# Kernel optimization log

Hardware: AMD Instinct MI355X
Metric: run time of the kernel (lower is better)

The kernel has to match this reference:

```python
import jax, jax.numpy as jnp
import numpy as np

TAU = [1, 2, 4, 8]
B, T, FC, FX = 128, 2048, 512, 512


def setup_inputs() -> dict:
    key = jax.random.key(0)
    k1, k2, k3, k4 = jax.random.split(key, 4)
    C = jax.random.normal(k1, (B, T, FC), dtype=jnp.float32)
    X = jax.random.normal(k2, (B, T, FX), dtype=jnp.float32)
    # one Linear(encoding_size -> context_size) per tau; torch weight layout [out, in]
    W = jax.random.normal(k3, (len(TAU), FC, FX), dtype=jnp.float32) * (1.0 / np.sqrt(FX))
    b = jax.random.normal(k4, (len(TAU), FC), dtype=jnp.float32) * 0.01
    return {"C": C, "X": X, "W": W, "b": b}


def _infonce(Ct, Xe, Wk, bk):
    # Ct: [B, Tt, fc], Xe: [B, Tt, fx]
    Xt = jnp.einsum('btf,gf->btg', Xe, Wk) + bk          # Linear: [B, Tt, fc]
    Z = jnp.einsum('itf,jtf->ijt', Ct, Xt)               # scores [B, B, Tt]
    Zmax = jnp.max(Z, axis=1, keepdims=True)             # [B, 1, Tt]
    lse = jnp.log(jnp.sum(jnp.exp(Z - Zmax), axis=1)) + Zmax[:, 0]  # [B, Tt]
    Zdiag = jnp.diagonal(Z, axis1=0, axis2=1).T          # Z[i,i,t] -> [B, Tt]
    return jnp.mean(Zdiag - lse)


def reference(C, X, W, b):
    losses = [_infonce(C[:, :-t], X[:, t:], W[k], b[k]) for k, t in enumerate(TAU)]
    return jnp.stack(losses)
```

## Files before the change

### kernel.cpp

```cpp
#include <hip/hip_runtime.h>
#include <math.h>

constexpr int Tn  = 2048;
constexpr int FCn = 512;
constexpr int FXn = 512;
constexpr int SXW = 72;
constexpr int SYC = 136;
constexpr int SZS = 132;

typedef __attribute__((ext_vector_type(8))) short  bf16x8;
typedef __attribute__((ext_vector_type(4))) float  f32x4;

__device__ __forceinline__ unsigned pk2(float a, float b) {
  return __builtin_amdgcn_perm(__float_as_uint(b), __float_as_uint(a), 0x07060302u);
}
__device__ __forceinline__ uint4 pack8(float4 a, float4 b) {
  uint4 rv;
  rv.x = pk2(a.x, a.y); rv.y = pk2(a.z, a.w);
  rv.z = pk2(b.x, b.y); rv.w = pk2(b.z, b.w);
  return rv;
}

__device__ __forceinline__ void gll16(const unsigned short* g, void* lds) {
  __builtin_amdgcn_global_load_lds(
      (const __attribute__((address_space(1))) unsigned int*)g,
      (__attribute__((address_space(3))) unsigned int*)lds, 16, 0, 0);
}

__global__ void zero4(float* out) {
  if (threadIdx.x < 4) out[threadIdx.x] = 0.0f;
}

__global__ void finalize4(float* out) {
  int k = threadIdx.x;
  if (k < 4) out[k] *= 1.0f / (128.0f * (float)(Tn - (1 << k)));
}

__global__ void tobf16(const float* __restrict__ s, unsigned short* __restrict__ d) {
  int i = blockIdx.x * 256 + threadIdx.x;
  float4 v = ((const float4*)s)[i];
  uint2 p; p.x = pk2(v.x, v.y); p.y = pk2(v.z, v.w);
  ((uint2*)d)[i] = p;
}

__global__ __launch_bounds__(256, 2)
void infonce_v9(const float* __restrict__ Cp, const unsigned short* __restrict__ Xb,
                const unsigned short* __restrict__ Wb, float* __restrict__ out)
{
  __shared__ __align__(16) unsigned char smem[67648];
  char* sm = (char*)smem;
  float* sZ   = (float*)sm;
  float* sRed = (float*)(sm + 67584);

  const int tid = threadIdx.x;
  const int l   = tid & 63;
  const int w   = tid >> 6;
  const int r   = l & 15;
  const int h   = l >> 4;
  const int jw  = w >> 1;
  const int gw  = w & 1;
  const int iw  = w >> 1;
  const int jw2 = w & 1;

  const int orig = blockIdx.x;
  const int xcd  = orig & 7;
  const int loc  = orig >> 3;
  const int wg   = (xcd < 4) ? (xcd * 1024 + loc) : (4096 + (xcd - 4) * 1023 + loc);
  const int k    = wg & 3;
  const int t    = wg >> 2;
  const int tau  = 1 << k;
  if (t >= Tn - tau) return;
  const int s = t + tau;

  const int sub = l >> 2;
  const int gsw = (l & 3) ^ ((l >> 3) & 3);
  const size_t xstr = (size_t)Tn * FXn;
  const unsigned short* xs0 = Xb + (size_t)(w * 32 + sub) * xstr
                              + (size_t)s * FXn + gsw * 8;
  const unsigned short* xs1 = xs0 + (size_t)16 * xstr;
  const unsigned short* wk  = Wb + (size_t)k * (FCn * FXn) + gsw * 8;
  const unsigned short* ws0 = wk  + (size_t)(w * 64 + sub) * FXn;
  const unsigned short* ws1 = ws0 + (size_t)16 * FXn;
  const unsigned short* ws2 = ws0 + (size_t)32 * FXn;
  const unsigned short* ws3 = ws0 + (size_t)48 * FXn;

  const size_t cstr = (size_t)Tn * FCn;
  const float* cr0 = Cp + (size_t)(iw * 64 +  0 + r) * cstr + (size_t)t * FCn;
  const float* cr1 = Cp + (size_t)(iw * 64 + 16 + r) * cstr + (size_t)t * FCn;
  const float* cr2 = Cp + (size_t)(iw * 64 + 32 + r) * cstr + (size_t)t * FCn;
  const float* cr3 = Cp + (size_t)(iw * 64 + 48 + r) * cstr + (size_t)t * FCn;

  f32x4 zacc[4][4];
#pragma unroll
  for (int a = 0; a < 4; ++a)
#pragma unroll
    for (int b = 0; b < 4; ++b) zacc[a][b] = f32x4{0.f, 0.f, 0.f, 0.f};

#define STG8(BUFC, XC) do { \
    char* _bb = sm + (BUFC) * 24576; \
    const size_t _xo = (size_t)(XC) * 32; \
    gll16(xs0 + _xo, _bb + (w * 2    ) * 1024); \
    gll16(xs1 + _xo, _bb + (w * 2 + 1) * 1024); \
    const size_t _wo = wgc + _xo; \
    gll16(ws0 + _wo, _bb + 8192 + (w * 4    ) * 1024); \
    gll16(ws1 + _wo, _bb + 8192 + (w * 4 + 1) * 1024); \
    gll16(ws2 + _wo, _bb + 8192 + (w * 4 + 2) * 1024); \
    gll16(ws3 + _wo, _bb + 8192 + (w * 4 + 3) * 1024); \
  } while (0)

#define MFY8(BUFC) do { \
    const char* _bx = sm + (BUFC) * 24576; \
    const char* _bw = _bx + 8192; \
    const int _gb = (h ^ ((r >> 1) & 3)) << 4; \
    bf16x8 _ax[4]; \
    _Pragma("unroll") \
    for (int _bm = 0; _bm < 4; ++_bm) \
      _ax[_bm] = *(const bf16x8*)(_bx + (jw * 64 + _bm * 16 + r) * 64 + _gb); \
    bf16x8 _bv[8]; \
    _Pragma("unroll") \
    for (int _bn = 0; _bn < 8; ++_bn) \
      _bv[_bn] = *(const bf16x8*)(_bw + (gw * 128 + _bn * 16 + r) * 64 + _gb); \
    _Pragma("unroll") \
    for (int _bm = 0; _bm < 4; ++_bm) \
      _Pragma("unroll") \
      for (int _bn = 0; _bn < 8; ++_bn) \
        yacc[_bm][_bn] = __builtin_amdgcn_mfma_f32_16x16x32_bf16( \
            _ax[_bm], _bv[_bn], yacc[_bm][_bn], 0, 0, 0); \
  } while (0)

#pragma unroll 1
  for (int gc = 0; gc < 2; ++gc) {
    const size_t wgc = (size_t)gc * 256 * FXn;
    f32x4 yacc[4][8];
#pragma unroll
    for (int a = 0; a < 4; ++a)
#pragma unroll
      for (int b = 0; b < 8; ++b) yacc[a][b] = f32x4{0.f, 0.f, 0.f, 0.f};

    STG8(0, 0);
    __syncthreads();
#pragma unroll 1
    for (int xc2 = 0; xc2 < 8; ++xc2) {
      STG8(1, 2 * xc2 + 1);
      MFY8(0);
      __syncthreads();
      if (xc2 < 7) STG8(0, 2 * xc2 + 2);
      MFY8(1);
      __syncthreads();
    }

#pragma unroll
    for (int bm = 0; bm < 4; ++bm)
#pragma unroll
      for (int bn = 0; bn < 8; ++bn)
#pragma unroll
        for (int reg = 0; reg < 4; ++reg) {
          const int row = jw * 64 + bm * 16 + h * 4 + reg;
          const int col = gw * 128 + bn * 16 + r;
          *(unsigned short*)(sm + row * 528 + col * 2) =
              (unsigned short)(__float_as_uint(yacc[bm][bn][reg]) >> 16);
        }
    __syncthreads();

#pragma unroll 2
    for (int ks2 = 0; ks2 < 8; ++ks2) {
      const int goff = gc * 256 + ks2 * 32 + h * 8;
      float4 u0 = *(const float4*)(cr0 + goff), p0 = *(const float4*)(cr0 + goff + 4);
      float4 u1 = *(const float4*)(cr1 + goff), p1 = *(const float4*)(cr1 + goff + 4);
      float4 u2 = *(const float4*)(cr2 + goff), p2 = *(const float4*)(cr2 + goff + 4);
      float4 u3 = *(const float4*)(cr3 + goff), p3 = *(const float4*)(cr3 + goff + 4);
      bf16x8 acv[4];
      acv[0] = __builtin_bit_cast(bf16x8, pack8(u0, p0));
      acv[1] = __builtin_bit_cast(bf16x8, pack8(u1, p1));
      acv[2] = __builtin_bit_cast(bf16x8, pack8(u2, p2));
      acv[3] = __builtin_bit_cast(bf16x8, pack8(u3, p3));
      const int gb = ks2 * 64 + h * 16;
      bf16x8 byv[4];
#pragma unroll
      for (int bn = 0; bn < 4; ++bn)
        byv[bn] = *(const bf16x8*)(sm + (jw2 * 64 + bn * 16 + r) * 528 + gb);
#pragma unroll
      for (int bm = 0; bm < 4; ++bm)
#pragma unroll
        for (int bn = 0; bn < 4; ++bn)
          zacc[bm][bn] = __builtin_amdgcn_mfma_f32_16x16x32_bf16(
              acv[bm], byv[bn], zacc[bm][bn], 0, 0, 0);
    }
    __syncthreads();
  }

#pragma unroll
  for (int bm = 0; bm < 4; ++bm)
#pragma unroll
    for (int bn = 0; bn < 4; ++bn)
#pragma unroll
      for (int reg = 0; reg < 4; ++reg)
        sZ[(iw * 64 + bm * 16 + h * 4 + reg) * SZS + (jw2 * 64 + bn * 16 + r)] =
            zacc[bm][bn][reg];
  __syncthreads();

  const int row = w * 32 + (l >> 1);
  const int c0l = l & 1;
  float mx = -3.4e38f;
#pragma unroll
  for (int m = 0; m < 64; ++m) mx = fmaxf(mx, sZ[row * SZS + c0l + m * 2]);
  mx = fmaxf(mx, __shfl_xor(mx, 1));
  float sum = 0.f;
#pragma unroll
  for (int m = 0; m < 64; ++m) sum += __expf(sZ[row * SZS + c0l + m * 2] - mx);
  sum += __shfl_xor(sum, 1);
  float val = (c0l == 0) ? (sZ[row * SZS + row] - (__logf(sum) + mx)) : 0.f;
#pragma unroll
  for (int off = 1; off < 64; off <<= 1) val += __shfl_xor(val, off);
  if (l == 0) sRed[w] = val;
  __syncthreads();
  if (tid == 0) atomicAdd(out + k, sRed[0] + sRed[1] + sRed[2] + sRed[3]);
#undef STG8
#undef MFY8
}

template <bool WBF>
__global__ __launch_bounds__(512, 4)
void infonce_main(const float* __restrict__ Cp, const float* __restrict__ Xp,
                  const void* __restrict__ Wp, float* __restrict__ out)
{
  __shared__ __align__(16) unsigned char smem[71680];
  unsigned short* sX = (unsigned short*)(smem);
  unsigned short* sW = (unsigned short*)(smem + 18432);
  unsigned short* sY = (unsigned short*)(smem + 36864);
  unsigned short* sC = (unsigned short*)(smem);
  float* sZ   = (float*)(smem);
  float* sRed = (float*)(smem + 67584);

  const int tid  = threadIdx.x;
  const int lane = tid & 63;
  const int wave = tid >> 6;
  const int r    = lane & 15;
  const int h    = lane >> 4;
  const int wr   = wave >> 1;
  const int wc   = wave & 1;

  const int orig = blockIdx.x;
  const int xcd  = orig & 7;
  const int loc  = orig >> 3;
  const int wg   = (xcd < 4) ? (xcd * 1024 + loc) : (4096 + (xcd - 4) * 1023 + loc);
  const int k    = wg & 3;
  const int t    = wg >> 2;
  const int tau  = 1 << k;
  if (t >= Tn - tau) return;

  const float* Cb = Cp + (size_t)t * FCn;
  const float* Xb = Xp + (size_t)(t + tau) * FXn;

  const int srow = tid >> 2;
  const int scol = (tid & 3) * 16;
  const float* xs = Xb + (size_t)srow * (Tn * FXn) + scol;
  unsigned short* xd = sX + srow * SXW + scol;
  unsigned short* wd = sW + srow * SXW + scol;
  const unsigned short* wsh = (const unsigned short*)Wp + (size_t)k * (FCn * FXn)
                              + (size_t)srow * FXn + scol;
  const float* wsf = (const float*)Wp + (size_t)k * (FCn * FXn)
                     + (size_t)srow * FXn + scol;
  const int crow0 = tid >> 4;
  const int ccol  = (tid & 15) * 8;
  const float* cs = Cb + (size_t)crow0 * (Tn * FCn) + ccol;
  unsigned short* cd = sC + crow0 * SYC + ccol;
  const size_t cstep = (size_t)32 * Tn * FCn;

  float4 px0, px1, px2, px3;
  float4 pw0, pw1, pw2, pw3;
  uint4  pb0, pb1;
  float4 pc0, pc1, pc2, pc3, pc4, pc5, pc6, pc7;

#define LOAD_X(XC) do { \
    const float4* _p = (const float4*)(xs + (XC) * 64); \
    px0 = _p[0]; px1 = _p[1]; px2 = _p[2]; px3 = _p[3]; } while (0)
#define LOAD_W(GC, XC) do { \
    if constexpr (WBF) { \
      const uint4* _p = (const uint4*)(wsh + (size_t)((GC) * 128) * FXn + (XC) * 64); \
      pb0 = _p[0]; pb1 = _p[1]; \
    } else { \
      const float4* _p = (const float4*)(wsf + (size_t)((GC) * 128) * FXn + (XC) * 64); \
      pw0 = _p[0]; pw1 = _p[1]; pw2 = _p[2]; pw3 = _p[3]; } } while (0)
#define STORE_XW() do { \
    *(uint4*)(xd)     = pack8(px0, px1); \
    *(uint4*)(xd + 8) = pack8(px2, px3); \
    if constexpr (WBF) { *(uint4*)(wd) = pb0; *(uint4*)(wd + 8) = pb1; } \
    else { *(uint4*)(wd) = pack8(pw0, pw1); *(uint4*)(wd + 8) = pack8(pw2, pw3); } \
  } while (0)
#define MFMA_YF() do { \
    _Pragma("unroll") \
    for (int ks = 0; ks < 2; ++ks) { \
      const int xoo = ks * 32 + h * 8; \
      bf16x8 a0 = *(const bf16x8*)(sX + (wr * 32 + 0  + r) * SXW + xoo); \
      bf16x8 a1 = *(const bf16x8*)(sX + (wr * 32 + 16 + r) * SXW + xoo); \
      _Pragma("unroll") \
      for (int bg = 0; bg < 4; ++bg) { \
        bf16x8 bb = *(const bf16x8*)(sW + (wc * 64 + bg * 16 + r) * SXW + xoo); \
        yacc[0][bg] = __builtin_amdgcn_mfma_f32_16x16x32_bf16(a0, bb, yacc[0][bg], 0, 0, 0); \
        yacc[1][bg] = __builtin_amdgcn_mfma_f32_16x16x32_bf16(a1, bb, yacc[1][bg], 0, 0, 0); \
      } } } while (0)

  f32x4 zacc[2][4];
#pragma unroll
  for (int a = 0; a < 2; ++a)
#pragma unroll
    for (int b = 0; b < 4; ++b) zacc[a][b] = f32x4{0.f, 0.f, 0.f, 0.f};

  LOAD_X(0); LOAD_W(0, 0);

  for (int gc = 0; gc < 4; ++gc) {
    f32x4 yacc[2][4];
#pragma unroll
    for (int a = 0; a < 2; ++a)
#pragma unroll
      for (int b = 0; b < 4; ++b) yacc[a][b] = f32x4{0.f, 0.f, 0.f, 0.f};

    for (int xc = 0; xc < 7; ++xc) {
      __syncthreads();
      STORE_XW();
      __syncthreads();
      LOAD_X(xc + 1); LOAD_W(gc, xc + 1);
      MFMA_YF();
    }
    __syncthreads();
    STORE_XW();
    __syncthreads();
    {
      const float4* p0 = (const float4*)(cs + 0 * cstep + gc * 128);
      const float4* p1 = (const float4*)(cs + 1 * cstep + gc * 128);
      const float4* p2 = (const float4*)(cs + 2 * cstep + gc * 128);
      const float4* p3 = (const float4*)(cs + 3 * cstep + gc * 128);
      pc0 = p0[0]; pc1 = p0[1];
      pc2 = p1[0]; pc3 = p1[1];
      pc4 = p2[0]; pc5 = p2[1];
      pc6 = p3[0]; pc7 = p3[1];
    }
    MFMA_YF();

#pragma unroll
    for (int aj = 0; aj < 2; ++aj)
#pragma unroll
      for (int bg = 0; bg < 4; ++bg)
#pragma unroll
        for (int reg = 0; reg < 4; ++reg)
          sY[(wr * 32 + aj * 16 + h * 4 + reg) * SYC + (wc * 64 + bg * 16 + r)] =
              (unsigned short)(__float_as_uint(yacc[aj][bg][reg]) >> 16);
    __syncthreads();
    *(uint4*)(cd + 0 * 32 * SYC) = pack8(pc0, pc1);
    *(uint4*)(cd + 1 * 32 * SYC) = pack8(pc2, pc3);
    *(uint4*)(cd + 2 * 32 * SYC) = pack8(pc4, pc5);
    *(uint4*)(cd + 3 * 32 * SYC) = pack8(pc6, pc7);
    __syncthreads();
    if (gc < 3) { LOAD_X(0); LOAD_W(gc + 1, 0); }
#pragma unroll
    for (int ks = 0; ks < 4; ++ks) {
      const int go = ks * 32 + h * 8;
      bf16x8 a0 = *(const bf16x8*)(sC + (wr * 32 + 0  + r) * SYC + go);
      bf16x8 a1 = *(const bf16x8*)(sC + (wr * 32 + 16 + r) * SYC + go);
#pragma unroll
      for (int bj = 0; bj < 4; ++bj) {
        bf16x8 bb = *(const bf16x8*)(sY + (wc * 64 + bj * 16 + r) * SYC + go);
        zacc[0][bj] = __builtin_amdgcn_mfma_f32_16x16x32_bf16(a0, bb, zacc[0][bj], 0, 0, 0);
        zacc[1][bj] = __builtin_amdgcn_mfma_f32_16x16x32_bf16(a1, bb, zacc[1][bj], 0, 0, 0);
      }
    }
  }
  __syncthreads();
#pragma unroll
  for (int ai = 0; ai < 2; ++ai)
#pragma unroll
    for (int bj = 0; bj < 4; ++bj)
#pragma unroll
      for (int reg = 0; reg < 4; ++reg)
        sZ[(wr * 32 + ai * 16 + h * 4 + reg) * SZS + (wc * 64 + bj * 16 + r)] =
            zacc[ai][bj][reg];
  __syncthreads();

  const int row = wave * 16 + (lane >> 2);
  const int c0l = lane & 3;
  float mx = -3.4e38f;
#pragma unroll
  for (int m = 0; m < 32; ++m) mx = fmaxf(mx, sZ[row * SZS + c0l + m * 4]);
  mx = fmaxf(mx, __shfl_xor(mx, 1));
  mx = fmaxf(mx, __shfl_xor(mx, 2));
  float sum = 0.f;
#pragma unroll
  for (int m = 0; m < 32; ++m) sum += __expf(sZ[row * SZS + c0l + m * 4] - mx);
  sum += __shfl_xor(sum, 1);
  sum += __shfl_xor(sum, 2);
  float val = (c0l == 0) ? (sZ[row * SZS + row] - (__logf(sum) + mx)) : 0.f;
#pragma unroll
  for (int off = 1; off < 64; off <<= 1) val += __shfl_xor(val, off);
  if (lane == 0) sRed[wave] = val;
  __syncthreads();
  if (tid == 0) {
    float bs = 0.f;
#pragma unroll
    for (int w2 = 0; w2 < 8; ++w2) bs += sRed[w2];
    atomicAdd(out + k, bs);
  }
#undef LOAD_X
#undef LOAD_W
#undef STORE_XW
#undef MFMA_YF
}

extern "C" void kernel_launch(void* const* d_in, const int* in_sizes, int n_in,
                              void* d_out, int out_size, void* d_ws, size_t ws_size,
                              hipStream_t stream) {
  const float* C = (const float*)d_in[0];
  const float* X = (const float*)d_in[1];
  const float* W = (const float*)d_in[2];
  float* out = (float*)d_out;

  const size_t NX = (size_t)128 * Tn * FXn;
  const size_t NW = (size_t)4 * FCn * FXn;
  const size_t WS_W   = NW * 2;
  const size_t WS_MID = WS_W + NX * 2;

  hipLaunchKernelGGL(zero4, dim3(1), dim3(64), 0, stream, out);

  if (ws_size >= WS_MID) {
    unsigned short* Wbf = (unsigned short*)d_ws;
    unsigned short* Xbf = (unsigned short*)((char*)d_ws + WS_W);
    hipLaunchKernelGGL(tobf16, dim3((unsigned)(NW / 1024)), dim3(256), 0, stream, W, Wbf);
    hipLaunchKernelGGL(tobf16, dim3((unsigned)(NX / 1024)), dim3(256), 0, stream, X, Xbf);
    hipLaunchKernelGGL(infonce_v9, dim3(2047 * 4), dim3(256), 0, stream,
                       C, Xbf, Wbf, out);
  } else if (ws_size >= WS_W) {
    hipLaunchKernelGGL(tobf16, dim3((unsigned)(NW / 1024)), dim3(256), 0, stream,
                       W, (unsigned short*)d_ws);
    hipLaunchKernelGGL(infonce_main<true>, dim3(2047 * 4), dim3(512), 0, stream,
                       C, X, (const void*)d_ws, out);
  } else {
    hipLaunchKernelGGL(infonce_main<false>, dim3(2047 * 4), dim3(512), 0, stream,
                       C, X, (const void*)W, out);
  }
  hipLaunchKernelGGL(finalize4, dim3(1), dim3(64), 0, stream, out);
}
```

Baseline: 1.532 ms.

## Split InfoNCE tile across eight waves and read X operands straight from global

The fused InfoNCE kernel now runs 512 threads (eight waves) per block instead of 256. Each wave owns a 32-row slice of the batch instead of 64, which halves the per-wave accumulator tiles. Only W is staged through LDS, in wider 64-column chunks with an XOR swizzle. X fragments are loaded directly from global memory into registers for the MFMA A operand, and the Y and softmax reductions are re-split across the extra waves. The aim is more latency hiding and less LDS staging traffic, at the cost of redundant global X reads by paired waves and fewer k-steps per synchronisation.

```diff
diff --git a/kernel.cpp b/kernel.cpp
--- a/kernel.cpp
+++ b/kernel.cpp
@@ -7,6 +7,7 @@
 constexpr int SXW = 72;
 constexpr int SYC = 136;
 constexpr int SZS = 132;
+constexpr int SYB = 520;
 
 typedef __attribute__((ext_vector_type(8))) short  bf16x8;
 typedef __attribute__((ext_vector_type(4))) float  f32x4;
@@ -43,9 +44,9 @@
   ((uint2*)d)[i] = p;
 }
 
-__global__ __launch_bounds__(256, 2)
-void infonce_v9(const float* __restrict__ Cp, const unsigned short* __restrict__ Xb,
-                const unsigned short* __restrict__ Wb, float* __restrict__ out)
+__global__ __launch_bounds__(512, 4)
+void infonce_v10(const float* __restrict__ Cp, const unsigned short* __restrict__ Xb,
+                 const unsigned short* __restrict__ Wb, float* __restrict__ out)
 {
   __shared__ __align__(16) unsigned char smem[67648];
   char* sm = (char*)smem;
@@ -72,151 +73,136 @@
   if (t >= Tn - tau) return;
   const int s = t + tau;
 
-  const int sub = l >> 2;
-  const int gsw = (l & 3) ^ ((l >> 3) & 3);
   const size_t xstr = (size_t)Tn * FXn;
-  const unsigned short* xs0 = Xb + (size_t)(w * 32 + sub) * xstr
-                              + (size_t)s * FXn + gsw * 8;
-  const unsigned short* xs1 = xs0 + (size_t)16 * xstr;
-  const unsigned short* wk  = Wb + (size_t)k * (FCn * FXn) + gsw * 8;
-  const unsigned short* ws0 = wk  + (size_t)(w * 64 + sub) * FXn;
-  const unsigned short* ws1 = ws0 + (size_t)16 * FXn;
-  const unsigned short* ws2 = ws0 + (size_t)32 * FXn;
-  const unsigned short* ws3 = ws0 + (size_t)48 * FXn;
+  const unsigned short* xr0 = Xb + (size_t)(jw * 32 +  0 + r) * xstr + (size_t)s * FXn;
+  const unsigned short* xr1 = xr0 + (size_t)16 * xstr;
+
+  const int gsw8 = ((l & 7) ^ (l >> 3)) * 8;
+  const unsigned short* wbase = Wb + (size_t)k * (FCn * FXn);
 
   const size_t cstr = (size_t)Tn * FCn;
-  const float* cr0 = Cp + (size_t)(iw * 64 +  0 + r) * cstr + (size_t)t * FCn;
-  const float* cr1 = Cp + (size_t)(iw * 64 + 16 + r) * cstr + (size_t)t * FCn;
-  const float* cr2 = Cp + (size_t)(iw * 64 + 32 + r) * cstr + (size_t)t * FCn;
-  const float* cr3 = Cp + (size_t)(iw * 64 + 48 + r) * cstr + (size_t)t * FCn;
-
-  f32x4 zacc[4][4];
-#pragma unroll
-  for (int a = 0; a < 4; ++a)
+  const float* cr0 = Cp + (size_t)(iw * 32 +  0 + r) * cstr + (size_t)t * FCn;
+  const float* cr1 = cr0 + (size_t)16 * cstr;
+
+  f32x4 zacc[2][4];
+#pragma unroll
+  for (int a = 0; a < 2; ++a)
 #pragma unroll
     for (int b = 0; b < 4; ++b) zacc[a][b] = f32x4{0.f, 0.f, 0.f, 0.f};
 
-#define STG8(BUFC, XC) do { \
-    char* _bb = sm + (BUFC) * 24576; \
-    const size_t _xo = (size_t)(XC) * 32; \
-    gll16(xs0 + _xo, _bb + (w * 2    ) * 1024); \
-    gll16(xs1 + _xo, _bb + (w * 2 + 1) * 1024); \
-    const size_t _wo = wgc + _xo; \
-    gll16(ws0 + _wo, _bb + 8192 + (w * 4    ) * 1024); \
-    gll16(ws1 + _wo, _bb + 8192 + (w * 4 + 1) * 1024); \
-    gll16(ws2 + _wo, _bb + 8192 + (w * 4 + 2) * 1024); \
-    gll16(ws3 + _wo, _bb + 8192 + (w * 4 + 3) * 1024); \
+#define STG10(BUF, GC, XC) do { \
+    char* _bb = sm + (BUF) * 32768 + (w * 32) * 128; \
+    const unsigned short* _ws = wbase \
+        + (size_t)((GC) * 256 + w * 32 + (l >> 3)) * FXn + (XC) * 64 + gsw8; \
+    gll16(_ws,                    _bb); \
+    gll16(_ws + (size_t)8  * FXn, _bb + 1024); \
+    gll16(_ws + (size_t)16 * FXn, _bb + 2048); \
+    gll16(_ws + (size_t)24 * FXn, _bb + 3072); \
   } while (0)
 
-#define MFY8(BUFC) do { \
-    const char* _bx = sm + (BUFC) * 24576; \
-    const char* _bw = _bx + 8192; \
-    const int _gb = (h ^ ((r >> 1) & 3)) << 4; \
-    bf16x8 _ax[4]; \
+#define MFY10(BUF, XC) do { \
+    const char* _bw = sm + (BUF) * 32768; \
     _Pragma("unroll") \
-    for (int _bm = 0; _bm < 4; ++_bm) \
-      _ax[_bm] = *(const bf16x8*)(_bx + (jw * 64 + _bm * 16 + r) * 64 + _gb); \
-    bf16x8 _bv[8]; \
-    _Pragma("unroll") \
-    for (int _bn = 0; _bn < 8; ++_bn) \
-      _bv[_bn] = *(const bf16x8*)(_bw + (gw * 128 + _bn * 16 + r) * 64 + _gb); \
-    _Pragma("unroll") \
-    for (int _bm = 0; _bm < 4; ++_bm) \
+    for (int _ks = 0; _ks < 2; ++_ks) { \
+      const int _xo = (XC) * 64 + _ks * 32 + h * 8; \
+      bf16x8 _a0 = *(const bf16x8*)(xr0 + _xo); \
+      bf16x8 _a1 = *(const bf16x8*)(xr1 + _xo); \
+      const int _cb = (_ks * 64 + h * 16) ^ ((r & 7) << 4); \
       _Pragma("unroll") \
-      for (int _bn = 0; _bn < 8; ++_bn) \
-        yacc[_bm][_bn] = __builtin_amdgcn_mfma_f32_16x16x32_bf16( \
-            _ax[_bm], _bv[_bn], yacc[_bm][_bn], 0, 0, 0); \
+      for (int _bn = 0; _bn < 8; ++_bn) { \
+        bf16x8 _bv = *(const bf16x8*)(_bw + (gw * 128 + _bn * 16 + r) * 128 + _cb); \
+        yacc[0][_bn] = __builtin_amdgcn_mfma_f32_16x16x32_bf16(_a0, _bv, yacc[0][_bn], 0, 0, 0); \
+        yacc[1][_bn] = __builtin_amdgcn_mfma_f32_16x16x32_bf16(_a1, _bv, yacc[1][_bn], 0, 0, 0); \
+      } \
+    } \
   } while (0)
 
 #pragma unroll 1
   for (int gc = 0; gc < 2; ++gc) {
-    const size_t wgc = (size_t)gc * 256 * FXn;
-    f32x4 yacc[4][8];
-#pragma unroll
-    for (int a = 0; a < 4; ++a)
+    f32x4 yacc[2][8];
+#pragma unroll
+    for (int a = 0; a < 2; ++a)
 #pragma unroll
       for (int b = 0; b < 8; ++b) yacc[a][b] = f32x4{0.f, 0.f, 0.f, 0.f};
 
-    STG8(0, 0);
+    STG10(0, gc, 0);
     __syncthreads();
 #pragma unroll 1
-    for (int xc2 = 0; xc2 < 8; ++xc2) {
-      STG8(1, 2 * xc2 + 1);
-      MFY8(0);
+    for (int p2 = 0; p2 < 4; ++p2) {
+      STG10(1, gc, 2 * p2 + 1);
+      MFY10(0, 2 * p2);
       __syncthreads();
-      if (xc2 < 7) STG8(0, 2 * xc2 + 2);
-      MFY8(1);
+      if (p2 < 3) STG10(0, gc, 2 * p2 + 2);
+      MFY10(1, 2 * p2 + 1);
       __syncthreads();
     }
 
 #pragma unroll
-    for (int bm = 0; bm < 4; ++bm)
+    for (int bm = 0; bm < 2; ++bm)
 #pragma unroll
       for (int bn = 0; bn < 8; ++bn)
 #pragma unroll
         for (int reg = 0; reg < 4; ++reg) {
-          const int row = jw * 64 + bm * 16 + h * 4 + reg;
+          const int row = jw * 32 + bm * 16 + h * 4 + reg;
           const int col = gw * 128 + bn * 16 + r;
-          *(unsigned short*)(sm + row * 528 + col * 2) =
+          *(unsigned short*)(sm + row * SYB + col * 2) =
               (unsigned short)(__float_as_uint(yacc[bm][bn][reg]) >> 16);
         }
     __syncthreads();
 
 #pragma unroll 2
     for (int ks2 = 0; ks2 < 8; ++ks2) {
-      const int goff = gc * 256 + ks2 * 32 + h * 8;
-      float4 u0 = *(const float4*)(cr0 + goff), p0 = *(const float4*)(cr0 + goff + 4);
-      float4 u1 = *(const float4*)(cr1 + goff), p1 = *(const float4*)(cr1 + goff + 4);
-      float4 u2 = *(const float4*)(cr2 + goff), p2 = *(const float4*)(cr2 + goff + 4);
-      float4 u3 = *(const float4*)(cr3 + goff), p3 = *(const float4*)(cr3 + goff + 4);
-      bf16x8 acv[4];
-      acv[0] = __builtin_bit_cast(bf16x8, pack8(u0, p0));
-      acv[1] = __builtin_bit_cast(bf16x8, pack8(u1, p1));
-      acv[2] = __builtin_bit_cast(bf16x8, pack8(u2, p2));
-      acv[3] = __builtin_bit_cast(bf16x8, pack8(u3, p3));
-      const int gb = ks2 * 64 + h * 16;
-      bf16x8 byv[4];
-#pragma unroll
-      for (int bn = 0; bn < 4; ++bn)
-        byv[bn] = *(const bf16x8*)(sm + (jw2 * 64 + bn * 16 + r) * 528 + gb);
-#pragma unroll
-      for (int bm = 0; bm < 4; ++bm)
-#pragma unroll
-        for (int bn = 0; bn < 4; ++bn)
-          zacc[bm][bn] = __builtin_amdgcn_mfma_f32_16x16x32_bf16(
-              acv[bm], byv[bn], zacc[bm][bn], 0, 0, 0);
+      const int gcol = gc * 256 + ks2 * 32 + h * 8;
+      float4 u0 = *(const float4*)(cr0 + gcol), p0 = *(const float4*)(cr0 + gcol + 4);
+      float4 u1 = *(const float4*)(cr1 + gcol), p1 = *(const float4*)(cr1 + gcol + 4);
+      bf16x8 a0 = __builtin_bit_cast(bf16x8, pack8(u0, p0));
+      bf16x8 a1 = __builtin_bit_cast(bf16x8, pack8(u1, p1));
+      const int yb = ks2 * 64 + h * 16;
+#pragma unroll
+      for (int bn = 0; bn < 4; ++bn) {
+        bf16x8 bv = *(const bf16x8*)(sm + (jw2 * 64 + bn * 16 + r) * SYB + yb);
+        zacc[0][bn] = __builtin_amdgcn_mfma_f32_16x16x32_bf16(a0, bv, zacc[0][bn], 0, 0, 0);
+        zacc[1][bn] = __builtin_amdgcn_mfma_f32_16x16x32_bf16(a1, bv, zacc[1][bn], 0, 0, 0);
+      }
     }
     __syncthreads();
   }
 
 #pragma unroll
-  for (int bm = 0; bm < 4; ++bm)
+  for (int bm = 0; bm < 2; ++bm)
 #pragma unroll
     for (int bn = 0; bn < 4; ++bn)
 #pragma unroll
       for (int reg = 0; reg < 4; ++reg)
-        sZ[(iw * 64 + bm * 16 + h * 4 + reg) * SZS + (jw2 * 64 + bn * 16 + r)] =
+        sZ[(iw * 32 + bm * 16 + h * 4 + reg) * SZS + (jw2 * 64 + bn * 16 + r)] =
             zacc[bm][bn][reg];
   __syncthreads();
 
-  const int row = w * 32 + (l >> 1);
-  const int c0l = l & 1;
+  const int row = w * 16 + (l >> 2);
+  const int c0l = l & 3;
   float mx = -3.4e38f;
 #pragma unroll
-  for (int m = 0; m < 64; ++m) mx = fmaxf(mx, sZ[row * SZS + c0l + m * 2]);
+  for (int m = 0; m < 32; ++m) mx = fmaxf(mx, sZ[row * SZS + c0l + m * 4]);
   mx = fmaxf(mx, __shfl_xor(mx, 1));
+  mx = fmaxf(mx, __shfl_xor(mx, 2));
   float sum = 0.f;
 #pragma unroll
-  for (int m = 0; m < 64; ++m) sum += __expf(sZ[row * SZS + c0l + m * 2] - mx);
+  for (int m = 0; m < 32; ++m) sum += __expf(sZ[row * SZS + c0l + m * 4] - mx);
   sum += __shfl_xor(sum, 1);
+  sum += __shfl_xor(sum, 2);
   float val = (c0l == 0) ? (sZ[row * SZS + row] - (__logf(sum) + mx)) : 0.f;
 #pragma unroll
   for (int off = 1; off < 64; off <<= 1) val += __shfl_xor(val, off);
   if (l == 0) sRed[w] = val;
   __syncthreads();
-  if (tid == 0) atomicAdd(out + k, sRed[0] + sRed[1] + sRed[2] + sRed[3]);
-#undef STG8
-#undef MFY8
+  if (tid == 0) {
+    float bs = 0.f;
+#pragma unroll
+    for (int w2 = 0; w2 < 8; ++w2) bs += sRed[w2];
+    atomicAdd(out + k, bs);
+  }
+#undef STG10
+#undef MFY10
 }
 
 template <bool WBF>
@@ -426,7 +412,7 @@
     unsigned short* Xbf = (unsigned short*)((char*)d_ws + WS_W);
     hipLaunchKernelGGL(tobf16, dim3((unsigned)(NW / 1024)), dim3(256), 0, stream, W, Wbf);
     hipLaunchKernelGGL(tobf16, dim3((unsigned)(NX / 1024)), dim3(256), 0, stream, X, Xbf);
-    hipLaunchKernelGGL(infonce_v9, dim3(2047 * 4), dim3(256), 0, stream,
+    hipLaunchKernelGGL(infonce_v10, dim3(2047 * 4), dim3(512), 0, stream,
                        C, Xbf, Wbf, out);
   } else if (ws_size >= WS_W) {
     hipLaunchKernelGGL(tobf16, dim3((unsigned)(NW / 1024)), dim3(256), 0, stream,
```

Result: slower. 2.170 ms (+41.7%).
